# Kernel tuning notes

Measured on AMD Instinct MI355X. Metric: run time of the kernel, lower is better.

Reference implementation:

```python
import jax, jax.numpy as jnp
import numpy as np

B, N, D, H = 8, 2048, 128, 4
DH = D // H
EPS_LN = 1e-5


def setup_inputs() -> dict:
    key = jax.random.key(0)
    ks = jax.random.split(key, 9)
    x = jax.random.normal(ks[0], (B, N, D), dtype=jnp.float32)
    u = jax.random.uniform(ks[1], (N, N), dtype=jnp.float32)
    adj = jnp.where(u > 0.5, u, 0.0)
    adj = adj.at[jnp.arange(N), jnp.arange(N)].set(1.0)
    W = jax.random.normal(ks[2], (D, D), dtype=jnp.float32) * (1.0 / np.sqrt(D))
    a_src = jax.random.normal(ks[3], (H, DH), dtype=jnp.float32) * 0.02
    a_dst = jax.random.normal(ks[4], (H, DH), dtype=jnp.float32) * 0.02
    Wo = jax.random.normal(ks[5], (D, D), dtype=jnp.float32) * (1.0 / np.sqrt(D))
    bo = jnp.zeros((D,), dtype=jnp.float32)
    gamma = jnp.ones((D,), dtype=jnp.float32)
    beta = jnp.zeros((D,), dtype=jnp.float32)
    return {"x": x, "adj_static": adj, "W": W, "a_src": a_src, "a_dst": a_dst,
            "Wo": Wo, "bo": bo, "gamma": gamma, "beta": beta}


def reference(x, adj_static, W, a_src, a_dst, Wo, bo, gamma, beta):
    # h: (B, H, N, DH)
    h = (x @ W.T).reshape(B, N, H, DH).transpose(0, 2, 1, 3)
    src = jnp.einsum('bhnd,hd->bhn', h, a_src)  # (B, H, N)
    dst = jnp.einsum('bhnd,hd->bhn', h, a_dst)  # (B, H, N)
    e = jax.nn.leaky_relu(src[..., :, None] + dst[..., None, :], 0.2)  # (B,H,N,N)
    logA = jnp.log(jnp.clip(adj_static, 1e-8))[None, None]
    mask = (adj_static > 0)[None, None]
    e = jnp.where(mask, e + logA, -jnp.inf)
    attn = jax.nn.softmax(e, axis=-1)  # dropout is identity in eval mode
    out = attn @ h  # (B, H, N, DH)
    out = out.transpose(0, 2, 1, 3).reshape(B, N, D)
    out = out @ Wo.T + bo
    y = x + out
    mu = jnp.mean(y, axis=-1, keepdims=True)
    var = jnp.mean(jnp.square(y - mu), axis=-1, keepdims=True)
    return (y - mu) * jax.lax.rsqrt(var + EPS_LN) * gamma + beta
```

## Files before the change

kernel.cpp:

```cpp
#include <hip/hip_runtime.h>

typedef short bf16x8 __attribute__((ext_vector_type(8)));
typedef float f32x4  __attribute__((ext_vector_type(4)));
typedef float f32x2  __attribute__((ext_vector_type(2)));
typedef int   i32x4  __attribute__((ext_vector_type(4)));
typedef unsigned int u32x2 __attribute__((ext_vector_type(2)));

#define DEV static __device__ __forceinline__
#define LOG2E 1.4426950408889634f

DEV float bfu_to_f(unsigned short s) { return __builtin_bit_cast(float, (unsigned int)s << 16); }
DEV unsigned short f_to_bf(float f) {
  unsigned int u = __builtin_bit_cast(unsigned int, f);
  u += 0x7fffu + ((u >> 16) & 1u);
  return (unsigned short)(u >> 16);
}
DEV unsigned int pack_bf_rne(float lo, float hi) {
  return (unsigned int)f_to_bf(lo) | ((unsigned int)f_to_bf(hi) << 16);
}
DEV unsigned int pack_bf_rtz(float lo, float hi) {
#if __has_builtin(__builtin_amdgcn_perm)
  return __builtin_amdgcn_perm(__builtin_bit_cast(unsigned int, hi),
                               __builtin_bit_cast(unsigned int, lo), 0x07060302u);
#else
  return (__builtin_bit_cast(unsigned int, hi) & 0xffff0000u) |
         (__builtin_bit_cast(unsigned int, lo) >> 16);
#endif
}
DEV float nexp2(float x) {
#if __has_builtin(__builtin_amdgcn_exp2f)
  return __builtin_amdgcn_exp2f(x);
#else
  return exp2f(x);
#endif
}

DEV bool detect_f32(const void* adj) { return ((const float*)adj)[0] == 1.0f; }

template<bool F32> DEV float ldS(const void* p, size_t i) {
  if constexpr (F32) return ((const float*)p)[i];
  else               return bfu_to_f(((const unsigned short*)p)[i]);
}
template<bool F32> DEV void ld8f(const void* p, size_t i, float* o) {
  if constexpr (F32) {
    const float* f = (const float*)p + i;
    f32x4 a = *(const f32x4*)f, b = *(const f32x4*)(f + 4);
    o[0]=a[0]; o[1]=a[1]; o[2]=a[2]; o[3]=a[3];
    o[4]=b[0]; o[5]=b[1]; o[6]=b[2]; o[7]=b[3];
  } else {
    i32x4 w = *(const i32x4*)((const unsigned short*)p + i);
#pragma unroll
    for (int k = 0; k < 4; ++k) {
      unsigned int u = (unsigned int)w[k];
      o[2*k]   = __builtin_bit_cast(float, u << 16);
      o[2*k+1] = __builtin_bit_cast(float, u & 0xffff0000u);
    }
  }
}
template<bool F32> DEV bf16x8 ldfrag(const void* p, size_t i) {
  if constexpr (F32) {
    float o[8]; ld8f<true>(p, i, o);
    union { bf16x8 v; unsigned short u[8]; } r;
#pragma unroll
    for (int k = 0; k < 8; ++k) r.u[k] = f_to_bf(o[k]);
    return r.v;
  } else {
    return __builtin_bit_cast(bf16x8, *(const i32x4*)((const unsigned short*)p + i));
  }
}

template<bool F32> DEV void k_h_body(const void* __restrict__ x, const void* __restrict__ W,
                                     unsigned short* __restrict__ hT,
                                     unsigned short (&t_s)[16][136]) {
  const int tid = threadIdx.x, lane = tid & 63, wave = tid >> 6;
  const int nt = blockIdx.x >> 3, ct = blockIdx.x & 7;
  const int m = lane & 15, q = lane >> 4;
  bf16x8 wf[4];
#pragma unroll
  for (int k = 0; k < 4; ++k)
    wf[k] = ldfrag<F32>(W, (size_t)(ct * 16 + m) * 128 + q * 8 + k * 32);
#pragma unroll
  for (int s = 0; s < 2; ++s) {
    const int nsub = wave * 2 + s;
    const size_t xr = (size_t)(nt * 128 + nsub * 16 + m) * 128 + q * 8;
    f32x4 acc = {0.f, 0.f, 0.f, 0.f};
#pragma unroll
    for (int k = 0; k < 4; ++k)
      acc = __builtin_amdgcn_mfma_f32_16x16x32_bf16(ldfrag<F32>(x, xr + k * 32), wf[k],
                                                    acc, 0, 0, 0);
    u32x2 w2; w2[0] = pack_bf_rne(acc[0], acc[1]); w2[1] = pack_bf_rne(acc[2], acc[3]);
    *(u32x2*)&t_s[m][nsub * 16 + q * 4] = w2;
  }
  __syncthreads();
  const int row = tid >> 4, c8 = tid & 15;
  const int chg = ct * 16 + row, hh = chg >> 5, dloc = chg & 31;
  const int ng = nt * 128 + c8 * 8, b = ng >> 11, nl = ng & 2047;
  i32x4 v = *(const i32x4*)&t_s[row][c8 * 8];
  *(i32x4*)(hT + ((size_t)((b * 4 + hh) * 32 + dloc)) * 2048 + nl) = v;
}
__global__ __launch_bounds__(256) void k_h(const void* x, const void* W,
                                           unsigned short* hT, const void* adj) {
  __shared__ __align__(16) unsigned short t_s[16][136];
  if (detect_f32(adj)) k_h_body<true>(x, W, hT, t_s); else k_h_body<false>(x, W, hT, t_s);
}

template<bool F32> DEV void k_sd_body(const unsigned short* __restrict__ hT,
                                      const void* __restrict__ a_src, const void* __restrict__ a_dst,
                                      float* __restrict__ srcv, float* __restrict__ dstv) {
  const int t = blockIdx.x * 256 + threadIdx.x;
  const int n = t & 2047, bh = t >> 11, hh = bh & 3;
  const unsigned short* col = hT + (size_t)bh * 32 * 2048 + n;
  float s = 0.f, d = 0.f;
#pragma unroll
  for (int dd = 0; dd < 32; ++dd) {
    const float v = bfu_to_f(col[(size_t)dd * 2048]);
    s += v * ldS<F32>(a_src, hh * 32 + dd);
    d += v * ldS<F32>(a_dst, hh * 32 + dd);
  }
  srcv[t] = s * LOG2E; dstv[t] = d * LOG2E;
}
__global__ __launch_bounds__(256) void k_sd(const unsigned short* hT, const void* a_src,
                                            const void* a_dst, float* srcv, float* dstv,
                                            const void* adj) {
  if (detect_f32(adj)) k_sd_body<true>(hT, a_src, a_dst, srcv, dstv);
  else                 k_sd_body<false>(hT, a_src, a_dst, srcv, dstv);
}

struct SmemAttn {
  unsigned short adj[2][64][132];
  unsigned short vt[2][2][32][132];
  float dst[2][2][128];
};

template<bool F32> DEV void k_attn_body(SmemAttn& sm, const void* __restrict__ adjv,
                                        const unsigned short* __restrict__ hT,
                                        const float* __restrict__ srcv,
                                        const float* __restrict__ dstv,
                                        unsigned short* __restrict__ ao) {
  const int tid = threadIdx.x, lane = tid & 63, wave = tid >> 6;
  const int bhp = blockIdx.x & 15, i64 = blockIdx.x >> 4;
  const int sub = wave >> 2, w4 = wave & 3;
  const int bh = bhp * 2 + sub;
  const int b = bh >> 2, hh = bh & 3;
  const int m = lane & 15, q = lane >> 4;
  const int i0 = i64 * 64;
  const int il = w4 * 16 + m;

  const int arow = tid >> 3, acol = (tid & 7) * 16;
  const int vsub = tid >> 8, vd = (tid >> 3) & 31, vcol = (tid & 7) * 16;
  const bool dstg = (tid & 7) == 0;
  const int dk = tid >> 3, dsub = dk >> 5, dj = (dk & 31) * 4;

  f32x4 fr[4];
  i32x4 br[2];
  i32x4 vr[2];
  f32x4 dr;

  {
    const size_t ga = (size_t)(i0 + arow) * 2048 + acol;
    i32x4 w0, w1;
    if constexpr (F32) {
#pragma unroll
      for (int p = 0; p < 4; ++p) fr[p] = *(const f32x4*)((const float*)adjv + ga + p * 4);
      w0[0]=(int)pack_bf_rtz(fr[0][0],fr[0][1]); w0[1]=(int)pack_bf_rtz(fr[0][2],fr[0][3]);
      w0[2]=(int)pack_bf_rtz(fr[1][0],fr[1][1]); w0[3]=(int)pack_bf_rtz(fr[1][2],fr[1][3]);
      w1[0]=(int)pack_bf_rtz(fr[2][0],fr[2][1]); w1[1]=(int)pack_bf_rtz(fr[2][2],fr[2][3]);
      w1[2]=(int)pack_bf_rtz(fr[3][0],fr[3][1]); w1[3]=(int)pack_bf_rtz(fr[3][2],fr[3][3]);
    } else {
      w0 = *(const i32x4*)((const unsigned short*)adjv + ga);
      w1 = *(const i32x4*)((const unsigned short*)adjv + ga + 8);
    }
    *(i32x4*)&sm.adj[0][arow][acol]     = w0;
    *(i32x4*)&sm.adj[0][arow][acol + 8] = w1;
    const unsigned short* vp = hT + ((size_t)((bhp * 2 + vsub) * 32 + vd)) * 2048 + vcol;
    *(i32x4*)&sm.vt[0][vsub][vd][vcol]     = *(const i32x4*)vp;
    *(i32x4*)&sm.vt[0][vsub][vd][vcol + 8] = *(const i32x4*)(vp + 8);
    if (dstg)
      *(f32x4*)&sm.dst[0][dsub][dj] = *(const f32x4*)(dstv + (size_t)(bhp * 2 + dsub) * 2048 + dj);
  }
  __syncthreads();

  const float src_i = srcv[bh * 2048 + i0 + il];
  const f32x2 src2 = {src_i, src_i};
  f32x4 acc0 = {0.f,0.f,0.f,0.f}, acc1 = {0.f,0.f,0.f,0.f};
  f32x4 acc2 = {0.f,0.f,0.f,0.f};
  i32x4 ones4;
  ones4[0] = ones4[1] = ones4[2] = ones4[3] = (int)0x3F803F80u;
  const bf16x8 Aones = __builtin_bit_cast(bf16x8, ones4);

  for (int c = 0; c < 16; ++c) {
    const int cb = c & 1;
    const bool pf = (c < 15);
    if (pf) {
      const int j1 = (c + 1) * 128;
      const size_t ga = (size_t)(i0 + arow) * 2048 + j1 + acol;
      if constexpr (F32) {
#pragma unroll
        for (int p = 0; p < 4; ++p) fr[p] = *(const f32x4*)((const float*)adjv + ga + p * 4);
      } else {
        br[0] = *(const i32x4*)((const unsigned short*)adjv + ga);
        br[1] = *(const i32x4*)((const unsigned short*)adjv + ga + 8);
      }
      const unsigned short* vp = hT + ((size_t)((bhp * 2 + vsub) * 32 + vd)) * 2048 + j1 + vcol;
      vr[0] = *(const i32x4*)vp;
      vr[1] = *(const i32x4*)(vp + 8);
      if (dstg)
        dr = *(const f32x4*)(dstv + (size_t)(bhp * 2 + dsub) * 2048 + j1 + dj);
    }
#pragma unroll
    for (int jc = 0; jc < 4; ++jc) {
      const int jq = jc * 32 + q * 8;
      i32x4 aw = *(const i32x4*)&sm.adj[cb][il][jq];
      f32x4 d0 = *(const f32x4*)&sm.dst[cb][sub][jq];
      f32x4 d1 = *(const f32x4*)&sm.dst[cb][sub][jq + 4];
      bf16x8 A0 = *(const bf16x8*)&sm.vt[cb][sub][m][jq];
      bf16x8 A1 = *(const bf16x8*)&sm.vt[cb][sub][16 + m][jq];
      i32x4 pk4;
#pragma unroll
      for (int t = 0; t < 4; ++t) {
        unsigned int w = (unsigned int)aw[t];
        f32x2 av;
        av[0] = __builtin_bit_cast(float, w << 16);
        av[1] = __builtin_bit_cast(float, w & 0xffff0000u);
        f32x2 dv;
        dv[0] = (t < 2) ? d0[2*t]     : d1[2*(t-2)];
        dv[1] = (t < 2) ? d0[2*t + 1] : d1[2*(t-2) + 1];
        const f32x2 sv = src2 + dv;
        const f32x2 lv = __builtin_elementwise_max(sv, 0.2f * sv);
        f32x2 ev; ev[0] = nexp2(lv[0]); ev[1] = nexp2(lv[1]);
        const f32x2 pv = av * ev;
        pk4[t] = (int)pack_bf_rtz(pv[0], pv[1]);
      }
      const bf16x8 pkv = __builtin_bit_cast(bf16x8, pk4);
      acc0 = __builtin_amdgcn_mfma_f32_16x16x32_bf16(A0, pkv, acc0, 0, 0, 0);
      acc1 = __builtin_amdgcn_mfma_f32_16x16x32_bf16(A1, pkv, acc1, 0, 0, 0);
      acc2 = __builtin_amdgcn_mfma_f32_16x16x32_bf16(Aones, pkv, acc2, 0, 0, 0);
    }
    if (pf) {
      const int nb = cb ^ 1;
      i32x4 w0, w1;
      if constexpr (F32) {
        w0[0]=(int)pack_bf_rtz(fr[0][0],fr[0][1]); w0[1]=(int)pack_bf_rtz(fr[0][2],fr[0][3]);
        w0[2]=(int)pack_bf_rtz(fr[1][0],fr[1][1]); w0[3]=(int)pack_bf_rtz(fr[1][2],fr[1][3]);
        w1[0]=(int)pack_bf_rtz(fr[2][0],fr[2][1]); w1[1]=(int)pack_bf_rtz(fr[2][2],fr[2][3]);
        w1[2]=(int)pack_bf_rtz(fr[3][0],fr[3][1]); w1[3]=(int)pack_bf_rtz(fr[3][2],fr[3][3]);
      } else { w0 = br[0]; w1 = br[1]; }
      *(i32x4*)&sm.adj[nb][arow][acol]     = w0;
      *(i32x4*)&sm.adj[nb][arow][acol + 8] = w1;
      *(i32x4*)&sm.vt[nb][vsub][vd][vcol]     = vr[0];
      *(i32x4*)&sm.vt[nb][vsub][vd][vcol + 8] = vr[1];
      if (dstg) *(f32x4*)&sm.dst[nb][dsub][dj] = dr;
    }
    __syncthreads();
  }

  const float inv = 1.f / fmaxf(acc2[0], 1e-20f);

  unsigned short* op = ao + ((size_t)(b * 2048) + i0 + il) * 128 + hh * 32 + q * 4;
  u32x2 w0, w1;
  w0[0] = pack_bf_rne(acc0[0] * inv, acc0[1] * inv);
  w0[1] = pack_bf_rne(acc0[2] * inv, acc0[3] * inv);
  w1[0] = pack_bf_rne(acc1[0] * inv, acc1[1] * inv);
  w1[1] = pack_bf_rne(acc1[2] * inv, acc1[3] * inv);
  *(u32x2*)op        = w0;
  *(u32x2*)(op + 16) = w1;
}
__global__ __launch_bounds__(512, 4) void k_attn(const void* adj, const unsigned short* hT,
                                                 const float* srcv, const float* dstv,
                                                 unsigned short* ao) {
  __shared__ __align__(16) SmemAttn sm;
  if (detect_f32(adj)) k_attn_body<true>(sm, adj, hT, srcv, dstv, ao);
  else                 k_attn_body<false>(sm, adj, hT, srcv, dstv, ao);
}

template<bool F32> DEV void k_out_body(const unsigned short* __restrict__ ao,
                                       const void* __restrict__ Wo, const void* __restrict__ bo,
                                       const void* __restrict__ x, const void* __restrict__ gamma,
                                       const void* __restrict__ beta, void* __restrict__ out,
                                       float (&y_s)[16][132]) {
  const int tid = threadIdx.x, lane = tid & 63, wave = tid >> 6;
  const int m = lane & 15, q = lane >> 4;
  const int rbase = blockIdx.x * 16;
  bf16x8 af[4];
#pragma unroll
  for (int k = 0; k < 4; ++k)
    af[k] = ldfrag<false>(ao, ((size_t)(rbase + m)) * 128 + q * 8 + k * 32);
  f32x4 acc[2] = {{0.f,0.f,0.f,0.f},{0.f,0.f,0.f,0.f}};
#pragma unroll
  for (int ct = 0; ct < 2; ++ct) {
    const size_t wrow = (size_t)(wave * 32 + ct * 16 + m) * 128 + q * 8;
#pragma unroll
    for (int k = 0; k < 4; ++k)
      acc[ct] = __builtin_amdgcn_mfma_f32_16x16x32_bf16(af[k], ldfrag<F32>(Wo, wrow + k * 32),
                                                        acc[ct], 0, 0, 0);
  }
#pragma unroll
  for (int ct = 0; ct < 2; ++ct) {
    const int c = wave * 32 + ct * 16 + m;
    const float bov = ldS<F32>(bo, c);
#pragma unroll
    for (int r = 0; r < 4; ++r) {
      const int row = q * 4 + r;
      y_s[row][c] = acc[ct][r] + bov + ldS<F32>(x, (size_t)(rbase + row) * 128 + c);
    }
  }
  __syncthreads();
  const int r = tid >> 4, c16 = tid & 15;
  float vals[8], sum = 0.f, sq = 0.f;
#pragma unroll
  for (int k = 0; k < 8; ++k) {
    const float v = y_s[r][c16 * 8 + k];
    vals[k] = v; sum += v; sq += v * v;
  }
#pragma unroll
  for (int msk = 1; msk < 16; msk <<= 1) {
    sum += __shfl_xor(sum, msk, 16);
    sq  += __shfl_xor(sq,  msk, 16);
  }
  const float mu  = sum * (1.f / 128.f);
  const float var = fmaxf(sq * (1.f / 128.f) - mu * mu, 0.f);
  const float rstd = rsqrtf(var + 1e-5f);
  float o[8];
#pragma unroll
  for (int k = 0; k < 8; ++k) {
    const int c = c16 * 8 + k;
    o[k] = (vals[k] - mu) * rstd * ldS<F32>(gamma, c) + ldS<F32>(beta, c);
  }
  const size_t obase = (size_t)(rbase + r) * 128 + c16 * 8;
  if constexpr (F32) {
    float* op = (float*)out + obase;
    f32x4 w0 = {o[0],o[1],o[2],o[3]}, w1 = {o[4],o[5],o[6],o[7]};
    *(f32x4*)op = w0; *(f32x4*)(op + 4) = w1;
  } else {
    union { unsigned short u[8]; i32x4 v; } ob;
#pragma unroll
    for (int k = 0; k < 8; ++k) ob.u[k] = f_to_bf(o[k]);
    *(i32x4*)((unsigned short*)out + obase) = ob.v;
  }
}
__global__ __launch_bounds__(256) void k_out(const unsigned short* ao, const void* Wo,
                                             const void* bo, const void* x, const void* gamma,
                                             const void* beta, void* out, const void* adj) {
  __shared__ __align__(16) float y_s[16][132];
  if (detect_f32(adj)) k_out_body<true>(ao, Wo, bo, x, gamma, beta, out, y_s);
  else                 k_out_body<false>(ao, Wo, bo, x, gamma, beta, out, y_s);
}

extern "C" void kernel_launch(void* const* d_in, const int* in_sizes, int n_in,
                              void* d_out, int out_size, void* d_ws, size_t ws_size,
                              hipStream_t stream) {
  const void* x     = d_in[0];
  const void* adj   = d_in[1];
  const void* W     = d_in[2];
  const void* a_src = d_in[3];
  const void* a_dst = d_in[4];
  const void* Wo    = d_in[5];
  const void* bo    = d_in[6];
  const void* gamma = d_in[7];
  const void* beta  = d_in[8];

  char* ws = (char*)d_ws;
  unsigned short* hT_ws  = (unsigned short*)ws;
  unsigned short* ao_ws  = (unsigned short*)(ws + 4194304);
  float*          src_ws = (float*)(ws + 8388608);
  float*          dst_ws = (float*)(ws + 8650752);

  k_h   <<<1024, 256, 0, stream>>>(x, W, hT_ws, adj);
  k_sd  <<<256,  256, 0, stream>>>(hT_ws, a_src, a_dst, src_ws, dst_ws, adj);
  k_attn<<<512,  512, 0, stream>>>(adj, hT_ws, src_ws, dst_ws, ao_ws);
  k_out <<<1024, 256, 0, stream>>>(ao_ws, Wo, bo, x, gamma, beta, d_out, adj);
}
```

Before: 166.9 us.

## Switch attention operands and V storage to FP8 with fp8 MFMA

Stores the projected features hT as FP8 instead of bf16, converts adjacency and unnormalized probabilities to FP8, and runs the attention-by-V and row-sum accumulations with 16x16x32 fp8 MFMA. This halves global and LDS traffic for V and adjacency tiles and raises the occupancy hint to 8 waves per EU. The cost is much lower precision: adjacency weights, exp values and h lose mantissa bits, and unscaled FP8 may underflow or saturate, which risks failing accuracy tolerances.

```diff
diff --git a/kernel.cpp b/kernel.cpp
--- a/kernel.cpp
+++ b/kernel.cpp
@@ -17,15 +17,6 @@
 }
 DEV unsigned int pack_bf_rne(float lo, float hi) {
   return (unsigned int)f_to_bf(lo) | ((unsigned int)f_to_bf(hi) << 16);
-}
-DEV unsigned int pack_bf_rtz(float lo, float hi) {
-#if __has_builtin(__builtin_amdgcn_perm)
-  return __builtin_amdgcn_perm(__builtin_bit_cast(unsigned int, hi),
-                               __builtin_bit_cast(unsigned int, lo), 0x07060302u);
-#else
-  return (__builtin_bit_cast(unsigned int, hi) & 0xffff0000u) |
-         (__builtin_bit_cast(unsigned int, lo) >> 16);
-#endif
 }
 DEV float nexp2(float x) {
 #if __has_builtin(__builtin_amdgcn_exp2f)
@@ -33,6 +24,13 @@
 #else
   return exp2f(x);
 #endif
+}
+template<bool HI> DEV unsigned int pk_fp8(float a, float b, unsigned int old) {
+  return __builtin_amdgcn_cvt_pk_fp8_f32(a, b, old, HI);
+}
+template<int W> DEV f32x2 upk_fp8(unsigned int w) {
+  auto r = __builtin_amdgcn_cvt_pk_f32_fp8(w, W);
+  f32x2 o; o[0] = r[0]; o[1] = r[1]; return o;
 }
 
 DEV bool detect_f32(const void* adj) { return ((const float*)adj)[0] == 1.0f; }
@@ -70,7 +68,7 @@
 }
 
 template<bool F32> DEV void k_h_body(const void* __restrict__ x, const void* __restrict__ W,
-                                     unsigned short* __restrict__ hT,
+                                     unsigned char* __restrict__ hT,
                                      unsigned short (&t_s)[16][136]) {
   const int tid = threadIdx.x, lane = tid & 63, wave = tid >> 6;
   const int nt = blockIdx.x >> 3, ct = blockIdx.x & 7;
@@ -96,30 +94,40 @@
   const int chg = ct * 16 + row, hh = chg >> 5, dloc = chg & 31;
   const int ng = nt * 128 + c8 * 8, b = ng >> 11, nl = ng & 2047;
   i32x4 v = *(const i32x4*)&t_s[row][c8 * 8];
-  *(i32x4*)(hT + ((size_t)((b * 4 + hh) * 32 + dloc)) * 2048 + nl) = v;
+  float f[8];
+#pragma unroll
+  for (int k = 0; k < 4; ++k) {
+    unsigned int u = (unsigned int)v[k];
+    f[2*k]   = __builtin_bit_cast(float, u << 16);
+    f[2*k+1] = __builtin_bit_cast(float, u & 0xffff0000u);
+  }
+  u32x2 o;
+  o[0] = pk_fp8<true>(f[2], f[3], pk_fp8<false>(f[0], f[1], 0u));
+  o[1] = pk_fp8<true>(f[6], f[7], pk_fp8<false>(f[4], f[5], 0u));
+  *(u32x2*)(hT + ((size_t)((b * 4 + hh) * 32 + dloc)) * 2048 + nl) = o;
 }
 __global__ __launch_bounds__(256) void k_h(const void* x, const void* W,
-                                           unsigned short* hT, const void* adj) {
+                                           unsigned char* hT, const void* adj) {
   __shared__ __align__(16) unsigned short t_s[16][136];
   if (detect_f32(adj)) k_h_body<true>(x, W, hT, t_s); else k_h_body<false>(x, W, hT, t_s);
 }
 
-template<bool F32> DEV void k_sd_body(const unsigned short* __restrict__ hT,
+template<bool F32> DEV void k_sd_body(const unsigned char* __restrict__ hT,
                                       const void* __restrict__ a_src, const void* __restrict__ a_dst,
                                       float* __restrict__ srcv, float* __restrict__ dstv) {
   const int t = blockIdx.x * 256 + threadIdx.x;
   const int n = t & 2047, bh = t >> 11, hh = bh & 3;
-  const unsigned short* col = hT + (size_t)bh * 32 * 2048 + n;
+  const unsigned char* col = hT + (size_t)bh * 32 * 2048 + n;
   float s = 0.f, d = 0.f;
 #pragma unroll
   for (int dd = 0; dd < 32; ++dd) {
-    const float v = bfu_to_f(col[(size_t)dd * 2048]);
+    const float v = __builtin_amdgcn_cvt_f32_fp8((int)col[(size_t)dd * 2048], 0);
     s += v * ldS<F32>(a_src, hh * 32 + dd);
     d += v * ldS<F32>(a_dst, hh * 32 + dd);
   }
   srcv[t] = s * LOG2E; dstv[t] = d * LOG2E;
 }
-__global__ __launch_bounds__(256) void k_sd(const unsigned short* hT, const void* a_src,
+__global__ __launch_bounds__(256) void k_sd(const unsigned char* hT, const void* a_src,
                                             const void* a_dst, float* srcv, float* dstv,
                                             const void* adj) {
   if (detect_f32(adj)) k_sd_body<true>(hT, a_src, a_dst, srcv, dstv);
@@ -127,13 +135,13 @@
 }
 
 struct SmemAttn {
-  unsigned short adj[2][64][132];
-  unsigned short vt[2][2][32][132];
+  unsigned char adj[2][64][144];
+  unsigned char vt[2][2][32][144];
   float dst[2][2][128];
 };
 
 template<bool F32> DEV void k_attn_body(SmemAttn& sm, const void* __restrict__ adjv,
-                                        const unsigned short* __restrict__ hT,
+                                        const unsigned char* __restrict__ hT,
                                         const float* __restrict__ srcv,
                                         const float* __restrict__ dstv,
                                         unsigned short* __restrict__ ao) {
@@ -153,28 +161,41 @@
 
   f32x4 fr[4];
   i32x4 br[2];
-  i32x4 vr[2];
+  i32x4 vr;
   f32x4 dr;
+
+  auto pack_adj = [&](i32x4& w) {
+    if constexpr (F32) {
+#pragma unroll
+      for (int p = 0; p < 4; ++p)
+        w[p] = (int)pk_fp8<true>(fr[p][2], fr[p][3], pk_fp8<false>(fr[p][0], fr[p][1], 0u));
+    } else {
+#pragma unroll
+      for (int p = 0; p < 4; ++p) {
+        unsigned int u0 = (unsigned int)br[p >> 1][(p & 1) * 2];
+        unsigned int u1 = (unsigned int)br[p >> 1][(p & 1) * 2 + 1];
+        const float f0 = __builtin_bit_cast(float, u0 << 16);
+        const float f1 = __builtin_bit_cast(float, u0 & 0xffff0000u);
+        const float f2 = __builtin_bit_cast(float, u1 << 16);
+        const float f3 = __builtin_bit_cast(float, u1 & 0xffff0000u);
+        w[p] = (int)pk_fp8<true>(f2, f3, pk_fp8<false>(f0, f1, 0u));
+      }
+    }
+  };
 
   {
     const size_t ga = (size_t)(i0 + arow) * 2048 + acol;
-    i32x4 w0, w1;
     if constexpr (F32) {
 #pragma unroll
       for (int p = 0; p < 4; ++p) fr[p] = *(const f32x4*)((const float*)adjv + ga + p * 4);
-      w0[0]=(int)pack_bf_rtz(fr[0][0],fr[0][1]); w0[1]=(int)pack_bf_rtz(fr[0][2],fr[0][3]);
-      w0[2]=(int)pack_bf_rtz(fr[1][0],fr[1][1]); w0[3]=(int)pack_bf_rtz(fr[1][2],fr[1][3]);
-      w1[0]=(int)pack_bf_rtz(fr[2][0],fr[2][1]); w1[1]=(int)pack_bf_rtz(fr[2][2],fr[2][3]);
-      w1[2]=(int)pack_bf_rtz(fr[3][0],fr[3][1]); w1[3]=(int)pack_bf_rtz(fr[3][2],fr[3][3]);
     } else {
-      w0 = *(const i32x4*)((const unsigned short*)adjv + ga);
-      w1 = *(const i32x4*)((const unsigned short*)adjv + ga + 8);
-    }
-    *(i32x4*)&sm.adj[0][arow][acol]     = w0;
-    *(i32x4*)&sm.adj[0][arow][acol + 8] = w1;
-    const unsigned short* vp = hT + ((size_t)((bhp * 2 + vsub) * 32 + vd)) * 2048 + vcol;
-    *(i32x4*)&sm.vt[0][vsub][vd][vcol]     = *(const i32x4*)vp;
-    *(i32x4*)&sm.vt[0][vsub][vd][vcol + 8] = *(const i32x4*)(vp + 8);
+      br[0] = *(const i32x4*)((const unsigned short*)adjv + ga);
+      br[1] = *(const i32x4*)((const unsigned short*)adjv + ga + 8);
+    }
+    vr = *(const i32x4*)(hT + ((size_t)((bhp * 2 + vsub) * 32 + vd)) * 2048 + vcol);
+    i32x4 w; pack_adj(w);
+    *(i32x4*)&sm.adj[0][arow][acol] = w;
+    *(i32x4*)&sm.vt[0][vsub][vd][vcol] = vr;
     if (dstg)
       *(f32x4*)&sm.dst[0][dsub][dj] = *(const f32x4*)(dstv + (size_t)(bhp * 2 + dsub) * 2048 + dj);
   }
@@ -184,9 +205,7 @@
   const f32x2 src2 = {src_i, src_i};
   f32x4 acc0 = {0.f,0.f,0.f,0.f}, acc1 = {0.f,0.f,0.f,0.f};
   f32x4 acc2 = {0.f,0.f,0.f,0.f};
-  i32x4 ones4;
-  ones4[0] = ones4[1] = ones4[2] = ones4[3] = (int)0x3F803F80u;
-  const bf16x8 Aones = __builtin_bit_cast(bf16x8, ones4);
+  const long Aones = 0x3838383838383838L;
 
   for (int c = 0; c < 16; ++c) {
     const int cb = c & 1;
@@ -201,54 +220,48 @@
         br[0] = *(const i32x4*)((const unsigned short*)adjv + ga);
         br[1] = *(const i32x4*)((const unsigned short*)adjv + ga + 8);
       }
-      const unsigned short* vp = hT + ((size_t)((bhp * 2 + vsub) * 32 + vd)) * 2048 + j1 + vcol;
-      vr[0] = *(const i32x4*)vp;
-      vr[1] = *(const i32x4*)(vp + 8);
+      vr = *(const i32x4*)(hT + ((size_t)((bhp * 2 + vsub) * 32 + vd)) * 2048 + j1 + vcol);
       if (dstg)
         dr = *(const f32x4*)(dstv + (size_t)(bhp * 2 + dsub) * 2048 + j1 + dj);
     }
 #pragma unroll
     for (int jc = 0; jc < 4; ++jc) {
       const int jq = jc * 32 + q * 8;
-      i32x4 aw = *(const i32x4*)&sm.adj[cb][il][jq];
+      u32x2 aw = *(const u32x2*)&sm.adj[cb][il][jq];
       f32x4 d0 = *(const f32x4*)&sm.dst[cb][sub][jq];
       f32x4 d1 = *(const f32x4*)&sm.dst[cb][sub][jq + 4];
-      bf16x8 A0 = *(const bf16x8*)&sm.vt[cb][sub][m][jq];
-      bf16x8 A1 = *(const bf16x8*)&sm.vt[cb][sub][16 + m][jq];
-      i32x4 pk4;
-#pragma unroll
-      for (int t = 0; t < 4; ++t) {
-        unsigned int w = (unsigned int)aw[t];
-        f32x2 av;
-        av[0] = __builtin_bit_cast(float, w << 16);
-        av[1] = __builtin_bit_cast(float, w & 0xffff0000u);
-        f32x2 dv;
-        dv[0] = (t < 2) ? d0[2*t]     : d1[2*(t-2)];
-        dv[1] = (t < 2) ? d0[2*t + 1] : d1[2*(t-2) + 1];
-        const f32x2 sv = src2 + dv;
-        const f32x2 lv = __builtin_elementwise_max(sv, 0.2f * sv);
-        f32x2 ev; ev[0] = nexp2(lv[0]); ev[1] = nexp2(lv[1]);
-        const f32x2 pv = av * ev;
-        pk4[t] = (int)pack_bf_rtz(pv[0], pv[1]);
-      }
-      const bf16x8 pkv = __builtin_bit_cast(bf16x8, pk4);
-      acc0 = __builtin_amdgcn_mfma_f32_16x16x32_bf16(A0, pkv, acc0, 0, 0, 0);
-      acc1 = __builtin_amdgcn_mfma_f32_16x16x32_bf16(A1, pkv, acc1, 0, 0, 0);
-      acc2 = __builtin_amdgcn_mfma_f32_16x16x32_bf16(Aones, pkv, acc2, 0, 0, 0);
+      long A0 = *(const long*)&sm.vt[cb][sub][m][jq];
+      long A1 = *(const long*)&sm.vt[cb][sub][16 + m][jq];
+      f32x2 av0 = upk_fp8<0>(aw[0]), av1 = upk_fp8<1>(aw[0]);
+      f32x2 av2 = upk_fp8<0>(aw[1]), av3 = upk_fp8<1>(aw[1]);
+      f32x2 dv0; dv0[0] = d0[0]; dv0[1] = d0[1];
+      f32x2 dv1; dv1[0] = d0[2]; dv1[1] = d0[3];
+      f32x2 dv2; dv2[0] = d1[0]; dv2[1] = d1[1];
+      f32x2 dv3; dv3[0] = d1[2]; dv3[1] = d1[3];
+      f32x2 sv0 = src2 + dv0, sv1 = src2 + dv1, sv2 = src2 + dv2, sv3 = src2 + dv3;
+      f32x2 lv0 = __builtin_elementwise_max(sv0, 0.2f * sv0);
+      f32x2 lv1 = __builtin_elementwise_max(sv1, 0.2f * sv1);
+      f32x2 lv2 = __builtin_elementwise_max(sv2, 0.2f * sv2);
+      f32x2 lv3 = __builtin_elementwise_max(sv3, 0.2f * sv3);
+      f32x2 ev0, ev1, ev2, ev3;
+      ev0[0] = nexp2(lv0[0]); ev0[1] = nexp2(lv0[1]);
+      ev1[0] = nexp2(lv1[0]); ev1[1] = nexp2(lv1[1]);
+      ev2[0] = nexp2(lv2[0]); ev2[1] = nexp2(lv2[1]);
+      ev3[0] = nexp2(lv3[0]); ev3[1] = nexp2(lv3[1]);
+      f32x2 pv0 = av0 * ev0, pv1 = av1 * ev1, pv2 = av2 * ev2, pv3 = av3 * ev3;
+      u32x2 bp;
+      bp[0] = pk_fp8<true>(pv1[0], pv1[1], pk_fp8<false>(pv0[0], pv0[1], 0u));
+      bp[1] = pk_fp8<true>(pv3[0], pv3[1], pk_fp8<false>(pv2[0], pv2[1], 0u));
+      const long B = __builtin_bit_cast(long, bp);
+      acc0 = __builtin_amdgcn_mfma_f32_16x16x32_fp8_fp8(A0, B, acc0, 0, 0, 0);
+      acc1 = __builtin_amdgcn_mfma_f32_16x16x32_fp8_fp8(A1, B, acc1, 0, 0, 0);
+      acc2 = __builtin_amdgcn_mfma_f32_16x16x32_fp8_fp8(Aones, B, acc2, 0, 0, 0);
     }
     if (pf) {
       const int nb = cb ^ 1;
-      i32x4 w0, w1;
-      if constexpr (F32) {
-        w0[0]=(int)pack_bf_rtz(fr[0][0],fr[0][1]); w0[1]=(int)pack_bf_rtz(fr[0][2],fr[0][3]);
-        w0[2]=(int)pack_bf_rtz(fr[1][0],fr[1][1]); w0[3]=(int)pack_bf_rtz(fr[1][2],fr[1][3]);
-        w1[0]=(int)pack_bf_rtz(fr[2][0],fr[2][1]); w1[1]=(int)pack_bf_rtz(fr[2][2],fr[2][3]);
-        w1[2]=(int)pack_bf_rtz(fr[3][0],fr[3][1]); w1[3]=(int)pack_bf_rtz(fr[3][2],fr[3][3]);
-      } else { w0 = br[0]; w1 = br[1]; }
-      *(i32x4*)&sm.adj[nb][arow][acol]     = w0;
-      *(i32x4*)&sm.adj[nb][arow][acol + 8] = w1;
-      *(i32x4*)&sm.vt[nb][vsub][vd][vcol]     = vr[0];
-      *(i32x4*)&sm.vt[nb][vsub][vd][vcol + 8] = vr[1];
+      i32x4 w; pack_adj(w);
+      *(i32x4*)&sm.adj[nb][arow][acol] = w;
+      *(i32x4*)&sm.vt[nb][vsub][vd][vcol] = vr;
       if (dstg) *(f32x4*)&sm.dst[nb][dsub][dj] = dr;
     }
     __syncthreads();
@@ -265,7 +278,7 @@
   *(u32x2*)op        = w0;
   *(u32x2*)(op + 16) = w1;
 }
-__global__ __launch_bounds__(512, 4) void k_attn(const void* adj, const unsigned short* hT,
+__global__ __launch_bounds__(512, 8) void k_attn(const void* adj, const unsigned char* hT,
                                                  const float* srcv, const float* dstv,
                                                  unsigned short* ao) {
   __shared__ __align__(16) SmemAttn sm;
@@ -360,10 +373,10 @@
   const void* beta  = d_in[8];
 
   char* ws = (char*)d_ws;
-  unsigned short* hT_ws  = (unsigned short*)ws;
-  unsigned short* ao_ws  = (unsigned short*)(ws + 4194304);
-  float*          src_ws = (float*)(ws + 8388608);
-  float*          dst_ws = (float*)(ws + 8650752);
+  unsigned char*  hT_ws  = (unsigned char*)ws;
+  unsigned short* ao_ws  = (unsigned short*)(ws + 2097152);
+  float*          src_ws = (float*)(ws + 6291456);
+  float*          dst_ws = (float*)(ws + 6553600);
 
   k_h   <<<1024, 256, 0, stream>>>(x, W, hT_ws, adj);
   k_sd  <<<256,  256, 0, stream>>>(hT_ws, a_src, a_dst, src_ws, dst_ws, adj);
```

Result: slower. 196.2 us (+17.5%).
